# Kernel tuning notes

Measured on AMD Instinct MI355X. Metric: run time of the kernel, lower is better.

## Reference

```python
import jax, jax.numpy as jnp
import numpy as np

F, H, D, A, B = 500, 2000, 64, 64, 4096


def setup_inputs() -> dict:
    key = jax.random.key(0)
    ks = jax.random.split(key, 6)
    values = jax.random.normal(ks[0], (B, F), dtype=jnp.float32)
    feat_emb = jax.random.normal(ks[1], (F, D), dtype=jnp.float32) * 0.02
    hid_emb = jax.random.normal(ks[2], (H, D), dtype=jnp.float32) * 0.02
    Ww = jax.random.normal(ks[3], (2 * D, A), dtype=jnp.float32) * (1.0 / np.sqrt(2 * D))
    bw = jnp.zeros((A,), dtype=jnp.float32)
    Wu = jax.random.normal(ks[4], (A, 1), dtype=jnp.float32) * (1.0 / np.sqrt(A))
    mask = jax.random.bernoulli(ks[5], 0.1, (F, F + H, 1))
    return {"values": values, "feat_emb": feat_emb, "hid_emb": hid_emb,
            "Ww": Ww, "bw": bw, "Wu": Wu, "mask": mask}


def reference(values, feat_emb, hid_emb, Ww, bw, Wu, mask):
    d = feat_emb.shape[1]
    # full embedding matrix: concat(feature, hidden) -> [F+H, d]
    full = jnp.concatenate([feat_emb, hid_emb], axis=0)
    # Dense(tanh) on concat([feat_emb tiled, full tiled], axis=2) == split-weight form:
    # avoids materializing the [F, F+H, 2d] concat tensor (same math).
    W1, W2 = Ww[:d], Ww[d:]
    pre_f = feat_emb @ W1          # [F, A]
    pre_w = full @ W2              # [F+H, A]
    h = jnp.tanh(pre_f[:, None, :] + pre_w[None, :, :] + bw)  # [F, F+H, A]
    score = h @ Wu                 # [F, F+H, 1]
    # masked exp-normalize (not a stable softmax: original uses raw exp)
    score = jnp.where(mask, jnp.exp(score), 0.0)
    ssum = jnp.sum(score, axis=1, keepdims=True)        # [F, 1, 1]
    ssum = jnp.where(ssum == 0, 1.0, ssum)
    attn = score / ssum                                  # [F, F+H, 1]
    context = jnp.sum(attn * full[None, :, :], axis=1)   # [F, d]
    return values @ context                              # [B, d]
```

## Files before the change

### kernel.cpp

```cpp
#include <hip/hip_runtime.h>
#include <cstdint>
#include <cstddef>

#define F_N 500
#define H_N 2000
#define JN  2500
#define D_N 64
#define A_N 64
#define B_N 4096

__global__ __launch_bounds__(256) void k_pre(
    const float* __restrict__ feat, const float* __restrict__ hid,
    const float* __restrict__ Ww,   const float* __restrict__ bw,
    float* __restrict__ pre_f, float* __restrict__ pre_w)
{
    const int lane = threadIdx.x & 63;
    const int wave = threadIdx.x >> 6;
    int row = blockIdx.x * 4 + wave;
    row = __builtin_amdgcn_readfirstlane(row);
    if (row >= F_N + JN) return;

    const float* emb;
    const float* W;
    float*       outp;
    float acc0, acc1 = 0.0f;

    if (row < F_N) {
        emb  = feat + (size_t)row * D_N;
        W    = Ww;
        outp = pre_f + (size_t)row * A_N;
        acc0 = bw[lane];
    } else {
        const int j = row - F_N;
        emb  = (j < F_N) ? (feat + (size_t)j * D_N)
                         : (hid + (size_t)(j - F_N) * D_N);
        W    = Ww + D_N * A_N;
        outp = pre_w + (size_t)j * A_N;
        acc0 = 0.0f;
    }

    #pragma unroll
    for (int d = 0; d < D_N; d += 2) {
        acc0 = fmaf(emb[d],     W[(d    ) * A_N + lane], acc0);
        acc1 = fmaf(emb[d + 1], W[(d + 1) * A_N + lane], acc1);
    }
    outp[lane] = acc0 + acc1;
}

__global__ __launch_bounds__(256) void k_attn(
    const float* __restrict__ feat, const float* __restrict__ hid,
    const float* __restrict__ pre_f, const float* __restrict__ pre_w,
    const float* __restrict__ Wu,   const void* __restrict__ mask,
    float* __restrict__ ctx)
{
    const int tid  = threadIdx.x;
    const int lane = tid & 63;
    const int wave = tid >> 6;
    const int i    = blockIdx.x;

    __shared__ int   list[JN];
    __shared__ float earr[JN];
    __shared__ float s_ctx[4][64];
    __shared__ int   nact;

    if (tid == 0) nact = 0;
    __syncthreads();

    const uint32_t* mw = (const uint32_t*)mask;
    const uint32_t probe = mw[lane] | mw[64 + lane] | mw[128 + lane] | mw[192 + lane];
    const bool byteMode = (__ballot(probe > 1u) != 0ull);

    const uint8_t*  mb = (const uint8_t*)mask + (size_t)i * JN;
    const uint32_t* mi = (const uint32_t*)mask + (size_t)i * JN;

    for (int t = tid; t < 2560; t += 256) {
        uint32_t m = 0;
        if (t < JN) m = byteMode ? (uint32_t)mb[t] : mi[t];
        const unsigned long long act = __ballot(m != 0);
        const int cnt = __popcll(act);
        int base = 0;
        if (lane == 0 && cnt) base = atomicAdd(&nact, cnt);
        base = __shfl(base, 0, 64);
        if (m) {
            const int rank = __popcll(act & ((1ull << lane) - 1ull));
            list[base + rank] = t;
        }
    }
    __syncthreads();
    const int n = nact;

    const float* pf = pre_f + (size_t)i * A_N;
    for (int idx = tid; idx < n; idx += 256) {
        const int j = list[idx];
        const float4* pwj = (const float4*)(pre_w + (size_t)j * A_N);
        float s = 0.0f;
        #pragma unroll
        for (int q = 0; q < 16; ++q) {
            const float4 v = pwj[q];
            const int a = q * 4;
            const float x0 = pf[a + 0] + v.x;
            const float x1 = pf[a + 1] + v.y;
            const float x2 = pf[a + 2] + v.z;
            const float x3 = pf[a + 3] + v.w;
            const float t0 = 1.0f - 2.0f / (__expf(2.0f * x0) + 1.0f);
            const float t1 = 1.0f - 2.0f / (__expf(2.0f * x1) + 1.0f);
            const float t2 = 1.0f - 2.0f / (__expf(2.0f * x2) + 1.0f);
            const float t3 = 1.0f - 2.0f / (__expf(2.0f * x3) + 1.0f);
            s = fmaf(Wu[a + 0], t0, s);
            s = fmaf(Wu[a + 1], t1, s);
            s = fmaf(Wu[a + 2], t2, s);
            s = fmaf(Wu[a + 3], t3, s);
        }
        earr[idx] = __expf(s);
    }
    __syncthreads();

    float cacc = 0.0f;
    int idx = wave;
    for (; idx + 12 < n; idx += 16) {
        const float e0 = earr[idx];      const int j0 = list[idx];
        const float e1 = earr[idx + 4];  const int j1 = list[idx + 4];
        const float e2 = earr[idx + 8];  const int j2 = list[idx + 8];
        const float e3 = earr[idx + 12]; const int j3 = list[idx + 12];
        const float* r0 = (j0 < F_N) ? (feat + (size_t)j0 * D_N) : (hid + (size_t)(j0 - F_N) * D_N);
        const float* r1 = (j1 < F_N) ? (feat + (size_t)j1 * D_N) : (hid + (size_t)(j1 - F_N) * D_N);
        const float* r2 = (j2 < F_N) ? (feat + (size_t)j2 * D_N) : (hid + (size_t)(j2 - F_N) * D_N);
        const float* r3 = (j3 < F_N) ? (feat + (size_t)j3 * D_N) : (hid + (size_t)(j3 - F_N) * D_N);
        const float v0 = r0[lane];
        const float v1 = r1[lane];
        const float v2 = r2[lane];
        const float v3 = r3[lane];
        cacc = fmaf(e0, v0, cacc);
        cacc = fmaf(e1, v1, cacc);
        cacc = fmaf(e2, v2, cacc);
        cacc = fmaf(e3, v3, cacc);
    }
    for (; idx < n; idx += 4) {
        const float e = earr[idx];
        const int   j = list[idx];
        const float* row = (j < F_N) ? (feat + (size_t)j * D_N)
                                     : (hid + (size_t)(j - F_N) * D_N);
        cacc = fmaf(e, row[lane], cacc);
    }
    s_ctx[wave][lane] = cacc;
    __syncthreads();

    if (wave == 0) {
        const float c4 = s_ctx[0][lane] + s_ctx[1][lane] + s_ctx[2][lane] + s_ctx[3][lane];
        float ss = 0.0f;
        for (int k = lane; k < n; k += 64) ss += earr[k];
        #pragma unroll
        for (int off = 1; off < 64; off <<= 1) ss += __shfl_xor(ss, off, 64);
        if (ss == 0.0f) ss = 1.0f;
        ctx[(size_t)i * D_N + lane] = c4 / ss;
    }
}

__global__ __launch_bounds__(256) void k_out(
    const float* __restrict__ values, const float* __restrict__ ctx,
    float* __restrict__ out)
{
    const int lane = threadIdx.x & 63;
    const int wave = threadIdx.x >> 6;
    const int row0 = blockIdx.x * 16 + wave * 4;

    __shared__ float lds[100 * 64];
    float acc0 = 0.0f, acc1 = 0.0f, acc2 = 0.0f, acc3 = 0.0f;

    for (int chunk = 0; chunk < 5; ++chunk) {
        const int k0 = chunk * 100;
        __syncthreads();
        for (int t = threadIdx.x; t < 100 * 64; t += 256)
            lds[t] = ctx[(size_t)k0 * 64 + t];
        __syncthreads();

        const float* v0p = values + (size_t)row0 * 500 + k0;
        const float* v1p = v0p + 500;
        const float* v2p = v0p + 1000;
        const float* v3p = v0p + 1500;
        #pragma unroll 5
        for (int kc = 0; kc < 100; kc += 4) {
            const float4 a = *(const float4*)(v0p + kc);
            const float4 b = *(const float4*)(v1p + kc);
            const float4 c = *(const float4*)(v2p + kc);
            const float4 d = *(const float4*)(v3p + kc);
            const float l0 = lds[(kc + 0) * 64 + lane];
            const float l1 = lds[(kc + 1) * 64 + lane];
            const float l2 = lds[(kc + 2) * 64 + lane];
            const float l3 = lds[(kc + 3) * 64 + lane];
            acc0 = fmaf(a.x, l0, acc0); acc0 = fmaf(a.y, l1, acc0);
            acc0 = fmaf(a.z, l2, acc0); acc0 = fmaf(a.w, l3, acc0);
            acc1 = fmaf(b.x, l0, acc1); acc1 = fmaf(b.y, l1, acc1);
            acc1 = fmaf(b.z, l2, acc1); acc1 = fmaf(b.w, l3, acc1);
            acc2 = fmaf(c.x, l0, acc2); acc2 = fmaf(c.y, l1, acc2);
            acc2 = fmaf(c.z, l2, acc2); acc2 = fmaf(c.w, l3, acc2);
            acc3 = fmaf(d.x, l0, acc3); acc3 = fmaf(d.y, l1, acc3);
            acc3 = fmaf(d.z, l2, acc3); acc3 = fmaf(d.w, l3, acc3);
        }
    }
    out[(size_t)(row0 + 0) * 64 + lane] = acc0;
    out[(size_t)(row0 + 1) * 64 + lane] = acc1;
    out[(size_t)(row0 + 2) * 64 + lane] = acc2;
    out[(size_t)(row0 + 3) * 64 + lane] = acc3;
}

extern "C" void kernel_launch(void* const* d_in, const int* in_sizes, int n_in,
                              void* d_out, int out_size, void* d_ws, size_t ws_size,
                              hipStream_t stream)
{
    const float* values = (const float*)d_in[0];
    const float* feat   = (const float*)d_in[1];
    const float* hid    = (const float*)d_in[2];
    const float* Ww     = (const float*)d_in[3];
    const float* bw     = (const float*)d_in[4];
    const float* Wu     = (const float*)d_in[5];
    const void*  mask   = d_in[6];
    float* out = (float*)d_out;

    float* wsf   = (float*)d_ws;
    float* pre_f = wsf;
    float* pre_w = wsf + 32000;
    float* ctx   = wsf + 192000;

    k_pre <<<750, 256, 0, stream>>>(feat, hid, Ww, bw, pre_f, pre_w);
    k_attn<<<500, 256, 0, stream>>>(feat, hid, pre_f, pre_w, Wu, mask, ctx);
    k_out <<<256, 256, 0, stream>>>(values, ctx, out);
}
```

Measured before the change: 136.7 us.

## Register-prefetch next ctx/values chunk and stage values tile in LDS for k_out

The output GEMM kernel now loads the next 100-row chunk of ctx and the block's values tile into registers while computing on the current chunk. Values are staged in shared memory, so the inner loop reads only LDS instead of issuing wave-uniform global float4 loads. This overlaps global latency with FMA work, at the cost of extra registers (nine float4 buffers) and extra LDS.

```diff
diff --git a/kernel.cpp b/kernel.cpp
--- a/kernel.cpp
+++ b/kernel.cpp
@@ -160,48 +160,103 @@
     const float* __restrict__ values, const float* __restrict__ ctx,
     float* __restrict__ out)
 {
-    const int lane = threadIdx.x & 63;
-    const int wave = threadIdx.x >> 6;
-    const int row0 = blockIdx.x * 16 + wave * 4;
-
-    __shared__ float lds[100 * 64];
+    const int tid  = threadIdx.x;
+    const int lane = tid & 63;
+    const int wave = tid >> 6;
+    const int rowB = blockIdx.x * 16;
+    const int r0   = wave * 4;
+
+    __shared__ float ctx_l[100 * 64];
+    __shared__ float vals_l[16 * 100];
+
+    float4 cbuf[7];
+    float4 vbuf[2];
+
     float acc0 = 0.0f, acc1 = 0.0f, acc2 = 0.0f, acc3 = 0.0f;
 
+    {
+        const float4* cp = (const float4*)(ctx);
+        #pragma unroll
+        for (int q = 0; q < 7; ++q) {
+            const int t = tid + q * 256;
+            if (t < 1600) cbuf[q] = cp[t];
+        }
+        #pragma unroll
+        for (int q = 0; q < 2; ++q) {
+            const int t = tid + q * 256;
+            if (t < 400) {
+                const int r = t / 25, c = t % 25;
+                vbuf[q] = *(const float4*)(values + (size_t)(rowB + r) * 500 + c * 4);
+            }
+        }
+    }
+
     for (int chunk = 0; chunk < 5; ++chunk) {
-        const int k0 = chunk * 100;
         __syncthreads();
-        for (int t = threadIdx.x; t < 100 * 64; t += 256)
-            lds[t] = ctx[(size_t)k0 * 64 + t];
+        {
+            float4* cl = (float4*)ctx_l;
+            #pragma unroll
+            for (int q = 0; q < 7; ++q) {
+                const int t = tid + q * 256;
+                if (t < 1600) cl[t] = cbuf[q];
+            }
+            float4* vl = (float4*)vals_l;
+            #pragma unroll
+            for (int q = 0; q < 2; ++q) {
+                const int t = tid + q * 256;
+                if (t < 400) vl[t] = vbuf[q];
+            }
+        }
         __syncthreads();
 
-        const float* v0p = values + (size_t)row0 * 500 + k0;
-        const float* v1p = v0p + 500;
-        const float* v2p = v0p + 1000;
-        const float* v3p = v0p + 1500;
+        if (chunk < 4) {
+            const int k0 = (chunk + 1) * 100;
+            const float4* cp = (const float4*)(ctx + (size_t)k0 * 64);
+            #pragma unroll
+            for (int q = 0; q < 7; ++q) {
+                const int t = tid + q * 256;
+                if (t < 1600) cbuf[q] = cp[t];
+            }
+            #pragma unroll
+            for (int q = 0; q < 2; ++q) {
+                const int t = tid + q * 256;
+                if (t < 400) {
+                    const int r = t / 25, c = t % 25;
+                    vbuf[q] = *(const float4*)(values + (size_t)(rowB + r) * 500 + k0 + c * 4);
+                }
+            }
+        }
+
+        const float* v0 = vals_l + (r0 + 0) * 100;
+        const float* v1 = vals_l + (r0 + 1) * 100;
+        const float* v2 = vals_l + (r0 + 2) * 100;
+        const float* v3 = vals_l + (r0 + 3) * 100;
         #pragma unroll 5
-        for (int kc = 0; kc < 100; kc += 4) {
-            const float4 a = *(const float4*)(v0p + kc);
-            const float4 b = *(const float4*)(v1p + kc);
-            const float4 c = *(const float4*)(v2p + kc);
-            const float4 d = *(const float4*)(v3p + kc);
-            const float l0 = lds[(kc + 0) * 64 + lane];
-            const float l1 = lds[(kc + 1) * 64 + lane];
-            const float l2 = lds[(kc + 2) * 64 + lane];
-            const float l3 = lds[(kc + 3) * 64 + lane];
-            acc0 = fmaf(a.x, l0, acc0); acc0 = fmaf(a.y, l1, acc0);
-            acc0 = fmaf(a.z, l2, acc0); acc0 = fmaf(a.w, l3, acc0);
-            acc1 = fmaf(b.x, l0, acc1); acc1 = fmaf(b.y, l1, acc1);
-            acc1 = fmaf(b.z, l2, acc1); acc1 = fmaf(b.w, l3, acc1);
-            acc2 = fmaf(c.x, l0, acc2); acc2 = fmaf(c.y, l1, acc2);
-            acc2 = fmaf(c.z, l2, acc2); acc2 = fmaf(c.w, l3, acc2);
-            acc3 = fmaf(d.x, l0, acc3); acc3 = fmaf(d.y, l1, acc3);
-            acc3 = fmaf(d.z, l2, acc3); acc3 = fmaf(d.w, l3, acc3);
-        }
-    }
-    out[(size_t)(row0 + 0) * 64 + lane] = acc0;
-    out[(size_t)(row0 + 1) * 64 + lane] = acc1;
-    out[(size_t)(row0 + 2) * 64 + lane] = acc2;
-    out[(size_t)(row0 + 3) * 64 + lane] = acc3;
+        for (int k = 0; k < 100; k += 4) {
+            const float4 a = *(const float4*)(v0 + k);
+            const float4 b = *(const float4*)(v1 + k);
+            const float4 c = *(const float4*)(v2 + k);
+            const float4 d = *(const float4*)(v3 + k);
+            const float c0 = ctx_l[(k + 0) * 64 + lane];
+            const float c1 = ctx_l[(k + 1) * 64 + lane];
+            const float c2 = ctx_l[(k + 2) * 64 + lane];
+            const float c3 = ctx_l[(k + 3) * 64 + lane];
+            acc0 = fmaf(a.x, c0, acc0); acc0 = fmaf(a.y, c1, acc0);
+            acc0 = fmaf(a.z, c2, acc0); acc0 = fmaf(a.w, c3, acc0);
+            acc1 = fmaf(b.x, c0, acc1); acc1 = fmaf(b.y, c1, acc1);
+            acc1 = fmaf(b.z, c2, acc1); acc1 = fmaf(b.w, c3, acc1);
+            acc2 = fmaf(c.x, c0, acc2); acc2 = fmaf(c.y, c1, acc2);
+            acc2 = fmaf(c.z, c2, acc2); acc2 = fmaf(c.w, c3, acc2);
+            acc3 = fmaf(d.x, c0, acc3); acc3 = fmaf(d.y, c1, acc3);
+            acc3 = fmaf(d.z, c2, acc3); acc3 = fmaf(d.w, c3, acc3);
+        }
+    }
+
+    const int gr = rowB + r0;
+    out[(size_t)(gr + 0) * 64 + lane] = acc0;
+    out[(size_t)(gr + 1) * 64 + lane] = acc1;
+    out[(size_t)(gr + 2) * 64 + lane] = acc2;
+    out[(size_t)(gr + 3) * 64 + lane] = acc3;
 }
 
 extern "C" void kernel_launch(void* const* d_in, const int* in_sizes, int n_in,
```

Result: faster. 129.0 us (-5.7%).
